# Kernel optimization log

Hardware: AMD Instinct MI355X
Metric: run time of the kernel (lower is better)

## Reference

```python
import jax, jax.numpy as jnp
import numpy as np
from jax import lax

DN = ('NCHW', 'OIHW', 'NCHW')


def squash(x):
    # x: [..., d]; squared-norm over last dim
    sq = jnp.sum(x * x, axis=-1, keepdims=True)
    return sq * x / ((1.0 + sq) * jnp.sqrt(sq))


def setup_inputs() -> dict:
    key = jax.random.key(0)
    ks = jax.random.split(key, 6)
    B = 512
    x = jax.random.normal(ks[0], (B, 1, 28, 28), dtype=jnp.float32)
    conv1_w = jax.random.normal(ks[1], (256, 1, 9, 9), dtype=jnp.float32) * 0.05
    conv1_b = jnp.zeros((256,), dtype=jnp.float32)
    conv2_w = jax.random.normal(ks[2], (256, 256, 9, 9), dtype=jnp.float32) * 0.02
    conv2_b = jnp.zeros((256,), dtype=jnp.float32)
    # W: [num_routes=1152, num_capsules=10, out_channels=16, in_channels=8]
    W = jax.random.normal(ks[3], (1152, 10, 16, 8), dtype=jnp.float32)
    return {"x": x, "conv1_w": conv1_w, "conv1_b": conv1_b,
            "conv2_w": conv2_w, "conv2_b": conv2_b, "W": W}


def reference(x, conv1_w, conv1_b, conv2_w, conv2_b, W):
    B = x.shape[0]
    # conv1 + ReLU: [B,1,28,28] -> [B,256,20,20]
    h = lax.conv_general_dilated(x, conv1_w, (1, 1), 'VALID', dimension_numbers=DN)
    h = jax.nn.relu(h + conv1_b[None, :, None, None])
    # primary capsule conv: [B,256,20,20] -> [B,256,6,6], stride 2
    h = lax.conv_general_dilated(h, conv2_w, (2, 2), 'VALID', dimension_numbers=DN)
    h = h + conv2_b[None, :, None, None]
    # reshape to capsules [B, 1152, 8] (matches torch .view on NCHW) and squash
    u = squash(h.reshape(B, -1, 8))
    # u_hat[b,r,c,o] = W[r,c,o,i] @ u[b,r,i]
    u_hat = jnp.einsum('rcoi,bri->brco', W, u)  # [B,1152,10,16]
    R, C = W.shape[0], W.shape[1]
    b_ij = jnp.zeros((R, C), dtype=x.dtype)
    num_iterations = 3
    for it in range(num_iterations):
        c_ij = jax.nn.softmax(b_ij, axis=0)          # softmax over routes
        s_j = jnp.einsum('rc,brco->bco', c_ij, u_hat)  # [B,10,16]
        v_j = squash(s_j)
        if it < num_iterations - 1:
            a_ij = jnp.einsum('brco,bco->brc', u_hat, v_j)  # agreement
            b_ij = b_ij + a_ij.mean(axis=0)
    return v_j  # [B,10,16]
```

## Files before the change

### kernel.cpp

```cpp
#include <hip/hip_runtime.h>
#include <stdint.h>


typedef unsigned short u16;
typedef unsigned int u32;
typedef _Float16 half8 __attribute__((ext_vector_type(8)));
typedef float f32x4 __attribute__((ext_vector_type(4)));

__device__ __forceinline__ u16 f2h(float f) {
  union { _Float16 h; u16 u; } cv;
  cv.h = (_Float16)f;
  return cv.u;
}

__device__ __forceinline__ void gload_lds16(const void* g, void* l) {
  __builtin_amdgcn_global_load_lds(
      (const __attribute__((address_space(1))) void*)g,
      (__attribute__((address_space(3))) void*)l, 16, 0, 0);
}

__global__ __launch_bounds__(256) void prologue_kernel(
    const float* __restrict__ x, const float* __restrict__ w1,
    const float* __restrict__ b1, const float* __restrict__ w2,
    const float* __restrict__ b2, u16* __restrict__ hT,
    u16* __restrict__ A2, float* __restrict__ u) {
  __shared__ __align__(16) char smraw[81 * 264 * 2];
  int bid = blockIdx.x;
  int tid = threadIdx.x;
  if (bid < 512) {
    float* xs = (float*)smraw;
    int b = bid;
    int co = tid;
    for (int i = co; i < 784; i += 256) xs[i] = x[(size_t)b * 784 + i];
    float w[81];
    const float* wp = w1 + co * 81;
#pragma unroll
    for (int k = 0; k < 81; ++k) w[k] = wp[k];
    float bias = b1[co];
    __syncthreads();
    u16* hb = hT + (size_t)b * 102400 + co;
    for (int yp = 0; yp < 10; ++yp) {
      int y0 = yp * 2;
      for (int g = 0; g < 5; ++g) {
        int xo = g * 4;
        float a0[4], a1[4];
#pragma unroll
        for (int j = 0; j < 4; ++j) { a0[j] = bias; a1[j] = bias; }
#pragma unroll
        for (int ky2 = 0; ky2 < 10; ++ky2) {
          const float* row = &xs[(y0 + ky2) * 28 + xo];
          float4 r0 = *(const float4*)row;
          float4 r1 = *(const float4*)(row + 4);
          float4 r2 = *(const float4*)(row + 8);
          float xr[12] = {r0.x, r0.y, r0.z, r0.w, r1.x, r1.y, r1.z, r1.w,
                          r2.x, r2.y, r2.z, r2.w};
          if (ky2 < 9) {
#pragma unroll
            for (int kx = 0; kx < 9; ++kx) {
              float wv = w[ky2 * 9 + kx];
              a0[0] = fmaf(wv, xr[kx], a0[0]);
              a0[1] = fmaf(wv, xr[kx + 1], a0[1]);
              a0[2] = fmaf(wv, xr[kx + 2], a0[2]);
              a0[3] = fmaf(wv, xr[kx + 3], a0[3]);
            }
          }
          if (ky2 >= 1) {
#pragma unroll
            for (int kx = 0; kx < 9; ++kx) {
              float wv = w[(ky2 - 1) * 9 + kx];
              a1[0] = fmaf(wv, xr[kx], a1[0]);
              a1[1] = fmaf(wv, xr[kx + 1], a1[1]);
              a1[2] = fmaf(wv, xr[kx + 2], a1[2]);
              a1[3] = fmaf(wv, xr[kx + 3], a1[3]);
            }
          }
        }
#pragma unroll
        for (int j = 0; j < 4; ++j) {
          hb[(y0 * 20 + xo + j) * 256] = f2h(fmaxf(a0[j], 0.f));
          hb[((y0 + 1) * 20 + xo + j) * 256] = f2h(fmaxf(a1[j], 0.f));
        }
      }
    }
  } else if (bid < 768) {
    u16* tl = (u16*)smraw;
    int co = bid - 512;
    const float* wp = w2 + (size_t)co * 20736;
#pragma unroll
    for (int k = 0; k < 81; ++k) {
      int li = k * 256 + tid;
      int ci = li / 81, t = li - ci * 81;
      tl[t * 264 + ci] = f2h(wp[li]);
    }
    __syncthreads();
    u16* op = A2 + (size_t)co * 20736;
    for (int oc = tid; oc < 2592; oc += 256) {
      int k0 = oc * 8;
      int t = k0 >> 8, ci0 = k0 & 255;
      *(uint4*)(op + k0) = *(const uint4*)&tl[t * 264 + ci0];
    }
  } else {
    int i = (bid - 768) * 256 + tid;
    int b = i / 2304, j0 = (i - b * 2304) * 4;
    float4 v;
    v.x = b2[j0 / 36]; v.y = b2[(j0 + 1) / 36];
    v.z = b2[(j0 + 2) / 36]; v.w = b2[(j0 + 3) / 36];
    *(float4*)(u + (size_t)b * 9216 + j0) = v;
  }
}

__global__ __launch_bounds__(512, 2) void conv2_kernel(
    const u16* __restrict__ hT, const u16* __restrict__ A2,
    float* __restrict__ u) {
  __shared__ __align__(16) u16 lds_[65536];
  char* const ldsc = (char*)lds_;
  const int bx = blockIdx.x;
  const int nbk = bx % 72, kz = bx / 72;
  const int n0 = nbk * 256;
  const int tid = threadIdx.x;
  const int lane = tid & 63, w = tid >> 6;
  const int wr = w >> 2, wc = w & 3;
  const int fr = lane & 15, fg = lane >> 4;
  const int w1024 = w * 1024;

  const int rA = tid >> 3;
  const int qsrc = (tid & 7) ^ (rA & 7);
  const int AbaseT = rA * 20736 + qsrc * 8;
  int Bb[4];
#pragma unroll
  for (int rg = 0; rg < 4; ++rg) {
    int n = n0 + rg * 64 + rA;
    int b = n / 36, sp = n - b * 36, oh = sp / 6, ow = sp - oh * 6;
    Bb[rg] = (b * 400 + oh * 40 + ow * 2) * 256 + qsrc * 8;
  }

  const int kx0 = (fg ^ (fr & 7)) << 4;
  const int kx1 = ((4 + fg) ^ (fr & 7)) << 4;
  const int wr16384 = wr * 16384;
  const int bh16384 = 32768 + (wc >> 1) * 16384;
  const int brow0 = (wc & 1) * 64;

  f32x4 acc[8][4] = {};
  half8 areg[4][2], breg[2][2][2];

#define STAGE_A(E, H, GT) do {                                               \
    char* p0_ = ldsc + (E) * 65536 + (H) * 8192 + w1024;                     \
    gload_lds16(A2 + AbaseT + (H) * 1327104 + (GT) * 64, p0_);               \
    char* p1_ = ldsc + (E) * 65536 + 16384 + (H) * 8192 + w1024;             \
    gload_lds16(A2 + AbaseT + (2 + (H)) * 1327104 + (GT) * 64, p1_);         \
  } while (0)
#define STAGE_B(E, H, BOFF) do {                                             \
    char* p_ = ldsc + (E) * 65536 + 32768 + (H) * 16384 + w1024;             \
    gload_lds16(hT + Bb[(H) * 2 + 0] + (BOFF), p_);                          \
    gload_lds16(hT + Bb[(H) * 2 + 1] + (BOFF), p_ + 8192);                   \
  } while (0)
#define RD_A(D, MH) do { _Pragma("unroll")                                   \
    for (int mr = 0; mr < 4; ++mr) {                                         \
      const char* r_ = ldsc + (D) * 65536 + wr16384 +                        \
                       ((MH) * 64 + mr * 16 + fr) * 128;                     \
      areg[mr][0] = *(const half8*)(r_ + kx0);                               \
      areg[mr][1] = *(const half8*)(r_ + kx1);                               \
    } } while (0)
#define RD_B(D, NH) do { _Pragma("unroll")                                   \
    for (int nr = 0; nr < 2; ++nr) {                                         \
      const char* r_ = ldsc + (D) * 65536 + bh16384 +                        \
                       (brow0 + (NH) * 32 + nr * 16 + fr) * 128;             \
      breg[NH][nr][0] = *(const half8*)(r_ + kx0);                           \
      breg[NH][nr][1] = *(const half8*)(r_ + kx1);                           \
    } } while (0)
#define MM16(MH, NH) do {                                                    \
    __builtin_amdgcn_s_setprio(1);                                           \
    _Pragma("unroll") for (int mr = 0; mr < 4; ++mr)                         \
    _Pragma("unroll") for (int nr = 0; nr < 2; ++nr) {                       \
      acc[(MH)*4+mr][(NH)*2+nr] = __builtin_amdgcn_mfma_f32_16x16x32_f16(    \
          areg[mr][0], breg[NH][nr][0], acc[(MH)*4+mr][(NH)*2+nr], 0, 0, 0); \
      acc[(MH)*4+mr][(NH)*2+nr] = __builtin_amdgcn_mfma_f32_16x16x32_f16(    \
          areg[mr][1], breg[NH][nr][1], acc[(MH)*4+mr][(NH)*2+nr], 0, 0, 0); \
    }                                                                        \
    __builtin_amdgcn_s_setprio(0);                                           \
  } while (0)
#define LGKM() do {                                                          \
    asm volatile("s_waitcnt lgkmcnt(0)" ::: "memory");                       \
    __builtin_amdgcn_sched_barrier(0);                                       \
  } while (0)
#define VM_BAR(N) do {                                                       \
    asm volatile("s_waitcnt vmcnt(" N ")" ::: "memory");                     \
    __builtin_amdgcn_s_barrier();                                            \
    asm volatile("" ::: "memory");                                           \
  } while (0)
#define TILE_STD2(T, D, E) do {                                              \
    const int gt_ = kz * 108 + (T) + 1;                                      \
    int tap_ = gt_ >> 2;                                                     \
    int kh_ = tap_ / 9, kw_ = tap_ - kh_ * 9;                                \
    int bo_ = (kh_ * 20 + kw_) * 256 + (gt_ & 3) * 64;                       \
    RD_A(D, 0); RD_B(D, 0); RD_B(D, 1);                                      \
    STAGE_A(E, 0, gt_); STAGE_B(E, 0, bo_); STAGE_B(E, 1, bo_);              \
    LGKM(); MM16(0, 0); MM16(0, 1); VM_BAR("6");                             \
    RD_A(D, 1);                                                              \
    STAGE_A(E, 1, gt_);                                                      \
    LGKM(); MM16(1, 0); MM16(1, 1); VM_BAR("2");                             \
  } while (0)
#define TILE_LAST2(D) do {                                                   \
    RD_A(D, 0); RD_B(D, 0); RD_B(D, 1);                                      \
    LGKM(); MM16(0, 0); MM16(0, 1); VM_BAR("0");                             \
    RD_A(D, 1);                                                              \
    LGKM(); MM16(1, 0); MM16(1, 1);                                          \
  } while (0)

  {
    const int gt0 = kz * 108;
    int tap = gt0 >> 2;
    int kh = tap / 9, kw = tap - kh * 9;
    int bo0 = (kh * 20 + kw) * 256 + (gt0 & 3) * 64;
    STAGE_A(0, 0, gt0); STAGE_B(0, 0, bo0); STAGE_B(0, 1, bo0);
    STAGE_A(0, 1, gt0);
    asm volatile("s_waitcnt vmcnt(2)" ::: "memory");
    __builtin_amdgcn_s_barrier();
    asm volatile("" ::: "memory");
  }
  for (int tt = 0; tt < 53; ++tt) {
    TILE_STD2(2 * tt, 0, 1);
    TILE_STD2(2 * tt + 1, 1, 0);
  }
  TILE_STD2(106, 0, 1);
  TILE_LAST2(1);

#pragma unroll
  for (int nf = 0; nf < 4; ++nf) {
    int cn = n0 + wc * 64 + nf * 16 + fr;
    int ob = cn / 36;
    int os = cn - ob * 36;
    float* op = u + (size_t)ob * 9216 + os;
#pragma unroll
    for (int mf = 0; mf < 8; ++mf) {
      int row0 = wr * 128 + mf * 16 + fg * 4;
#pragma unroll
      for (int qq = 0; qq < 4; ++qq)
        atomicAdd(op + (row0 + qq) * 36, acc[mf][nf][qq]);
    }
  }
#undef STAGE_A
#undef STAGE_B
#undef RD_A
#undef RD_B
#undef MM16
#undef LGKM
#undef VM_BAR
#undef TILE_STD2
#undef TILE_LAST2
}

__global__ __launch_bounds__(256) void squash_kernel(
    float* __restrict__ u, u16* __restrict__ ub) {
  int idx = blockIdx.x * 256 + threadIdx.x;
  float* up = u + (size_t)idx * 8;
  float4 a = *(const float4*)up;
  float4 c = *(const float4*)(up + 4);
  float sq = a.x * a.x + a.y * a.y + a.z * a.z + a.w * a.w +
             c.x * c.x + c.y * c.y + c.z * c.z + c.w * c.w;
  float f = sqrtf(sq) / (1.0f + sq);
  a.x *= f; a.y *= f; a.z *= f; a.w *= f;
  c.x *= f; c.y *= f; c.z *= f; c.w *= f;
  *(float4*)up = a;
  *(float4*)(up + 4) = c;
  u16 o[8];
  o[0] = f2h(a.x); o[1] = f2h(a.y); o[2] = f2h(a.z); o[3] = f2h(a.w);
  o[4] = f2h(c.x); o[5] = f2h(c.y); o[6] = f2h(c.z); o[7] = f2h(c.w);
  *(uint4*)(ub + (size_t)idx * 8) = *(uint4*)o;
}

__global__ __launch_bounds__(256) void transp_kernel(
    const u16* __restrict__ ub, u16* __restrict__ ubT) {
  __shared__ u16 tl[64][72];
  int ri0 = blockIdx.x * 64, b0 = blockIdx.y * 64;
  int tid = threadIdx.x;
  int br = tid >> 2, cq = tid & 3;
  const u16* ip = ub + (size_t)(b0 + br) * 9216 + ri0 + cq * 16;
  uint4 v0 = *(const uint4*)ip;
  uint4 v1 = *(const uint4*)(ip + 8);
  *(uint4*)&tl[br][cq * 16] = v0;
  *(uint4*)&tl[br][cq * 16 + 8] = v1;
  __syncthreads();
  int rr = tid >> 2, cb = tid & 3;
  u16 o0[8], o1[8];
#pragma unroll
  for (int j = 0; j < 8; ++j) {
    o0[j] = tl[cb * 16 + j][rr];
    o1[j] = tl[cb * 16 + 8 + j][rr];
  }
  u16* opp = ubT + (size_t)(ri0 + rr) * 512 + b0 + cb * 16;
  *(uint4*)opp = *(uint4*)o0;
  *(uint4*)(opp + 8) = *(uint4*)o1;
}

__global__ __launch_bounds__(256) void softmax_c_kernel(
    const float* __restrict__ bij, float* __restrict__ cT) {
  int c = blockIdx.x;
  int tid = threadIdx.x;
  __shared__ float red[256];
  float mx = -1e30f;
  for (int r = tid; r < 1152; r += 256) mx = fmaxf(mx, bij[r * 10 + c]);
  red[tid] = mx;
  __syncthreads();
  for (int s = 128; s > 0; s >>= 1) {
    if (tid < s) red[tid] = fmaxf(red[tid], red[tid + s]);
    __syncthreads();
  }
  mx = red[0];
  __syncthreads();
  float sum = 0.f;
  for (int r = tid; r < 1152; r += 256) sum += expf(bij[r * 10 + c] - mx);
  red[tid] = sum;
  __syncthreads();
  for (int s = 128; s > 0; s >>= 1) {
    if (tid < s) red[tid] += red[tid + s];
    __syncthreads();
  }
  float inv = 1.0f / red[0];
  for (int r = tid; r < 1152; r += 256)
    cT[c * 1152 + r] = expf(bij[r * 10 + c] - mx) * inv;
}

__global__ __launch_bounds__(256) void gemm_s_kernel(
    const float* __restrict__ W, const float* __restrict__ cT,
    const u16* __restrict__ ub, float* __restrict__ s) {
  __shared__ __align__(16) u16 Asl[160 * 72];
  __shared__ __align__(16) u16 Bsl[64 * 72];
  int nb = blockIdx.x & 7, kzi = blockIdx.x >> 3;
  int n0 = nb * 64, k0 = kzi * 256;
  int tid = threadIdx.x;
  int lane = tid & 63, wave = tid >> 6;
  int fr = lane & 15, fg = lane >> 4;

  f32x4 acc[10] = {};
#pragma unroll
  for (int st = 0; st < 4; ++st) {
    int kb = k0 + st * 64;
    __syncthreads();
#pragma unroll
    for (int j = 0; j < 5; ++j) {
      int c5 = tid + j * 256;
      int row = c5 >> 3, qq = c5 & 7;
      int cls = row >> 4, o = row & 15;
      int r = (kb + qq * 8) >> 3;
      const float* wp = W + (size_t)r * 1280 + cls * 128 + o * 8;
      float4 w0 = *(const float4*)wp;
      float4 w1 = *(const float4*)(wp + 4);
      float cs = cT[cls * 1152 + r] * 512.0f;
      u16 ov[8];
      ov[0] = f2h(w0.x * cs); ov[1] = f2h(w0.y * cs);
      ov[2] = f2h(w0.z * cs); ov[3] = f2h(w0.w * cs);
      ov[4] = f2h(w1.x * cs); ov[5] = f2h(w1.y * cs);
      ov[6] = f2h(w1.z * cs); ov[7] = f2h(w1.w * cs);
      *(uint4*)((char*)Asl + row * 144 + qq * 16) = *(uint4*)ov;
    }
#pragma unroll
    for (int j = 0; j < 2; ++j) {
      int c2 = tid + j * 256;
      int row = c2 >> 3, qq = c2 & 7;
      *(uint4*)((char*)Bsl + row * 144 + qq * 16) =
          *(const uint4*)(ub + (size_t)(n0 + row) * 9216 + kb + qq * 8);
    }
    __syncthreads();
#pragma unroll
    for (int s2 = 0; s2 < 2; ++s2) {
      int xg = (s2 * 4 + fg) * 16;
      half8 bf0 = *(const half8*)((char*)Bsl + (wave * 16 + fr) * 144 + xg);
#pragma unroll
      for (int m = 0; m < 10; ++m) {
        half8 af = *(const half8*)((char*)Asl + (m * 16 + fr) * 144 + xg);
        acc[m] = __builtin_amdgcn_mfma_f32_16x16x32_f16(af, bf0, acc[m], 0, 0, 0);
      }
    }
  }
  int bcol = n0 + wave * 16 + fr;
#pragma unroll
  for (int m = 0; m < 10; ++m)
#pragma unroll
    for (int qq = 0; qq < 4; ++qq)
      atomicAdd(s + (m * 16 + fg * 4 + qq) * 512 + bcol, acc[m][qq]);
}

__global__ __launch_bounds__(256) void squash_v_kernel(
    float* __restrict__ s, u16* __restrict__ vb) {
  int idx = blockIdx.x * 256 + threadIdx.x;
  int c = idx >> 9, b = idx & 511;
  float vals[16];
  float sq = 0.f;
#pragma unroll
  for (int o = 0; o < 16; ++o) {
    float v = s[(c * 16 + o) * 512 + b] * (1.0f / 512.0f);
    vals[o] = v;
    sq += v * v;
  }
#pragma unroll
  for (int o = 0; o < 16; ++o) s[(c * 16 + o) * 512 + b] = 0.f;
  float f = sqrtf(sq) / (1.0f + sq);
#pragma unroll
  for (int o = 0; o < 16; ++o)
    vb[(c * 16 + o) * 512 + b] = f2h(vals[o] * f * 4096.0f);
}

__global__ __launch_bounds__(256) void gemm_gc_kernel(
    const u16* __restrict__ vb, const u16* __restrict__ ubT,
    const float* __restrict__ W, float* __restrict__ bij) {
  __shared__ __align__(16) u16 Agl[160 * 72];
  __shared__ __align__(16) u16 Bgl[128 * 72];
  __shared__ float Gl[160 * 129];
  int nb = blockIdx.x % 72, kzi = blockIdx.x / 72;
  int n0 = nb * 128, k0 = kzi * 128;
  int tid = threadIdx.x;
  int lane = tid & 63, wave = tid >> 6;
  int fr = lane & 15, fg = lane >> 4;
  f32x4 acc[10][2] = {};
#pragma unroll
  for (int st = 0; st < 2; ++st) {
    int kb = k0 + st * 64;
    __syncthreads();
#pragma unroll
    for (int j = 0; j < 5; ++j) {
      int c5 = tid + j * 256;
      int row = c5 >> 3, qq = c5 & 7;
      *(uint4*)((char*)Agl + row * 144 + qq * 16) =
          *(const uint4*)(vb + (size_t)row * 512 + kb + qq * 8);
    }
#pragma unroll
    for (int j = 0; j < 4; ++j) {
      int c4 = tid + j * 256;
      int row = c4 >> 3, qq = c4 & 7;
      *(uint4*)((char*)Bgl + row * 144 + qq * 16) =
          *(const uint4*)(ubT + (size_t)(n0 + row) * 512 + kb + qq * 8);
    }
    __syncthreads();
#pragma unroll
    for (int s2 = 0; s2 < 2; ++s2) {
      int xg = (s2 * 4 + fg) * 16;
      half8 bfv[2];
#pragma unroll
      for (int nn = 0; nn < 2; ++nn)
        bfv[nn] = *(const half8*)((char*)Bgl + (wave * 32 + nn * 16 + fr) * 144 + xg);
#pragma unroll
      for (int m = 0; m < 10; ++m) {
        half8 af = *(const half8*)((char*)Agl + (m * 16 + fr) * 144 + xg);
#pragma unroll
        for (int nn = 0; nn < 2; ++nn)
          acc[m][nn] = __builtin_amdgcn_mfma_f32_16x16x32_f16(af, bfv[nn],
                                                             acc[m][nn], 0, 0, 0);
      }
    }
  }
#pragma unroll
  for (int m = 0; m < 10; ++m)
#pragma unroll
    for (int nn = 0; nn < 2; ++nn) {
      int col = wave * 32 + nn * 16 + fr;
#pragma unroll
      for (int qq = 0; qq < 4; ++qq)
        Gl[(m * 16 + fg * 4 + qq) * 129 + col] = acc[m][nn][qq];
    }
  __syncthreads();
  if (tid < 160) {
    int rl = tid / 10, c = tid - rl * 10;
    int r = (n0 >> 3) + rl;
    const float* wp = W + (size_t)r * 1280 + c * 128;
    float a = 0.f;
#pragma unroll 4
    for (int o = 0; o < 16; ++o) {
      const float* gp = &Gl[(c * 16 + o) * 129 + rl * 8];
#pragma unroll
      for (int i = 0; i < 8; ++i) a = fmaf(wp[o * 8 + i], gp[i], a);
    }
    atomicAdd(&bij[r * 10 + c], a * (1.0f / (512.0f * 4096.0f)));
  }
}

__global__ __launch_bounds__(256) void route_final_kernel(
    const float* __restrict__ cT, const float* __restrict__ u,
    const float* __restrict__ W, float* __restrict__ outp) {
  int c = blockIdx.y, b0 = blockIdx.x * 16;
  int tid = threadIdx.x, lb = tid >> 4, o = tid & 15;
  __shared__ float us[16][32][8];
  __shared__ float cs[32];
  float acc = 0.f;
  for (int r0 = 0; r0 < 1152; r0 += 32) {
    __syncthreads();
#pragma unroll
    for (int j = 0; j < 4; ++j) {
      int i4 = tid + j * 256;
      int bb = i4 >> 6, rem = i4 & 63;
      int rr = rem >> 1, hf = rem & 1;
      *(float4*)&us[bb][rr][hf * 4] =
          *(const float4*)&u[(size_t)(b0 + bb) * 9216 + (r0 + rr) * 8 + hf * 4];
    }
    if (tid < 32) cs[tid] = cT[c * 1152 + r0 + tid];
    __syncthreads();
#pragma unroll 4
    for (int rr = 0; rr < 32; ++rr) {
      const float* wp = W + ((size_t)(r0 + rr) * 10 + c) * 128 + o * 8;
      float4 w0 = *(const float4*)wp;
      float4 w1v = *(const float4*)(wp + 4);
      float4 ua = *(const float4*)&us[lb][rr][0];
      float4 ub4 = *(const float4*)&us[lb][rr][4];
      float d = w0.x * ua.x + w0.y * ua.y + w0.z * ua.z + w0.w * ua.w +
                w1v.x * ub4.x + w1v.y * ub4.y + w1v.z * ub4.z + w1v.w * ub4.w;
      acc = fmaf(cs[rr], d, acc);
    }
  }
  float sq = acc * acc;
  sq += __shfl_xor(sq, 1, 64);
  sq += __shfl_xor(sq, 2, 64);
  sq += __shfl_xor(sq, 4, 64);
  sq += __shfl_xor(sq, 8, 64);
  float f = sqrtf(sq) / (1.0f + sq);
  outp[((size_t)(b0 + lb) * 10 + c) * 16 + o] = acc * f;
}

extern "C" void kernel_launch(void* const* d_in, const int* in_sizes, int n_in,
                              void* d_out, int out_size, void* d_ws, size_t ws_size,
                              hipStream_t stream) {
  const float* x  = (const float*)d_in[0];
  const float* w1 = (const float*)d_in[1];
  const float* b1 = (const float*)d_in[2];
  const float* w2 = (const float*)d_in[3];
  const float* b2 = (const float*)d_in[4];
  const float* W  = (const float*)d_in[5];
  char* ws = (char*)d_ws;
  u16*   hT  = (u16*)ws;
  u16*   A2  = (u16*)(ws + 104857600);
  float* u   = (float*)(ws + 115474432);
  float* bij = (float*)(ws + 134348800);
  float* cT  = (float*)(ws + 134394880);
  float* s   = (float*)(ws + 134440960);
  u16*   ub  = (u16*)ws;
  u16*   ubT = (u16*)(ws + 9437184);
  u16*   vb  = (u16*)(ws + 21823488);
  float* out = (float*)d_out;

  hipMemsetAsync(bij, 0, 46080, stream);
  hipMemsetAsync(s, 0, 327680, stream);
  prologue_kernel<<<5376, 256, 0, stream>>>(x, w1, b1, w2, b2, hT, A2, u);
  conv2_kernel<<<216, 512, 0, stream>>>(hT, A2, u);
  squash_kernel<<<2304, 256, 0, stream>>>(u, ub);
  transp_kernel<<<dim3(144, 8), 256, 0, stream>>>(ub, ubT);
  for (int it = 0; it < 3; ++it) {
    softmax_c_kernel<<<10, 256, 0, stream>>>(bij, cT);
    if (it < 2) {
      gemm_s_kernel<<<288, 256, 0, stream>>>(W, cT, ub, s);
      squash_v_kernel<<<20, 256, 0, stream>>>(s, vb);
      gemm_gc_kernel<<<288, 256, 0, stream>>>(vb, ubT, W, bij);
    } else {
      route_final_kernel<<<dim3(32, 10), 256, 0, stream>>>(cT, u, W, out);
    }
  }
}
```

Baseline: 613.8 us.

## Double conv2 workgroup to 1024 threads with smaller per-wave tiles

The conv2 implicit GEMM moves from 512 to 1024 threads per block. Each of the 16 waves now computes a 64x64 output tile with 4x4 accumulators instead of 128x64, and each thread stages four 16-byte loads per K tile. The split two-phase pipeline with partial vmcnt waits is replaced by a simpler one that waits for all loads (vmcnt(0)) before each barrier. The aim is more waves for latency hiding and lower register pressure per wave. The cost is less MFMA work per LDS read and fully serialized waits on global loads at every tile.

Result: no change. 614.4 us (+0.1%).

```diff
diff --git a/kernel.cpp b/kernel.cpp
--- a/kernel.cpp
+++ b/kernel.cpp
@@ -109,7 +109,7 @@
   }
 }
 
-__global__ __launch_bounds__(512, 2) void conv2_kernel(
+__global__ __launch_bounds__(1024, 4) void conv2_kernel(
     const u16* __restrict__ hT, const u16* __restrict__ A2,
     float* __restrict__ u) {
   __shared__ __align__(16) u16 lds_[65536];
@@ -124,106 +124,86 @@
   const int w1024 = w * 1024;
 
   const int rA = tid >> 3;
-  const int qsrc = (tid & 7) ^ (rA & 7);
-  const int AbaseT = rA * 20736 + qsrc * 8;
-  int Bb[4];
-#pragma unroll
-  for (int rg = 0; rg < 4; ++rg) {
-    int n = n0 + rg * 64 + rA;
+  const int qs = (tid & 7) ^ (rA & 7);
+  const int Aoff0 = rA * 20736 + qs * 8;
+  const int Aoff1 = (128 + rA) * 20736 + qs * 8;
+  int Bb0, Bb1;
+  {
+    int n = n0 + rA;
     int b = n / 36, sp = n - b * 36, oh = sp / 6, ow = sp - oh * 6;
-    Bb[rg] = (b * 400 + oh * 40 + ow * 2) * 256 + qsrc * 8;
+    Bb0 = (b * 400 + oh * 40 + ow * 2) * 256 + qs * 8;
+    n = n0 + 128 + rA;
+    b = n / 36; sp = n - b * 36; oh = sp / 6; ow = sp - oh * 6;
+    Bb1 = (b * 400 + oh * 40 + ow * 2) * 256 + qs * 8;
   }
 
   const int kx0 = (fg ^ (fr & 7)) << 4;
   const int kx1 = ((4 + fg) ^ (fr & 7)) << 4;
-  const int wr16384 = wr * 16384;
-  const int bh16384 = 32768 + (wc >> 1) * 16384;
-  const int brow0 = (wc & 1) * 64;
-
-  f32x4 acc[8][4] = {};
-  half8 areg[4][2], breg[2][2][2];
-
-#define STAGE_A(E, H, GT) do {                                               \
-    char* p0_ = ldsc + (E) * 65536 + (H) * 8192 + w1024;                     \
-    gload_lds16(A2 + AbaseT + (H) * 1327104 + (GT) * 64, p0_);               \
-    char* p1_ = ldsc + (E) * 65536 + 16384 + (H) * 8192 + w1024;             \
-    gload_lds16(A2 + AbaseT + (2 + (H)) * 1327104 + (GT) * 64, p1_);         \
-  } while (0)
-#define STAGE_B(E, H, BOFF) do {                                             \
-    char* p_ = ldsc + (E) * 65536 + 32768 + (H) * 16384 + w1024;             \
-    gload_lds16(hT + Bb[(H) * 2 + 0] + (BOFF), p_);                          \
-    gload_lds16(hT + Bb[(H) * 2 + 1] + (BOFF), p_ + 8192);                   \
-  } while (0)
-#define RD_A(D, MH) do { _Pragma("unroll")                                   \
-    for (int mr = 0; mr < 4; ++mr) {                                         \
-      const char* r_ = ldsc + (D) * 65536 + wr16384 +                        \
-                       ((MH) * 64 + mr * 16 + fr) * 128;                     \
-      areg[mr][0] = *(const half8*)(r_ + kx0);                               \
-      areg[mr][1] = *(const half8*)(r_ + kx1);                               \
-    } } while (0)
-#define RD_B(D, NH) do { _Pragma("unroll")                                   \
-    for (int nr = 0; nr < 2; ++nr) {                                         \
-      const char* r_ = ldsc + (D) * 65536 + bh16384 +                        \
-                       (brow0 + (NH) * 32 + nr * 16 + fr) * 128;             \
-      breg[NH][nr][0] = *(const half8*)(r_ + kx0);                           \
-      breg[NH][nr][1] = *(const half8*)(r_ + kx1);                           \
-    } } while (0)
-#define MM16(MH, NH) do {                                                    \
+  const int arow = wr * 64 + fr;
+  const int brow = wc * 64 + fr;
+
+  f32x4 acc[4][4] = {};
+  half8 areg[4], breg[4];
+
+#define STAGE4(E, GT) do {                                                   \
+    int tap_ = (GT) >> 2;                                                    \
+    int kh_ = tap_ / 9, kw_ = tap_ - kh_ * 9;                                \
+    int bo_ = (kh_ * 20 + kw_) * 256 + ((GT) & 3) * 64;                      \
+    char* base_ = ldsc + (E) * 65536;                                        \
+    gload_lds16(A2 + Aoff0 + (GT) * 64, base_ + w1024);                      \
+    gload_lds16(A2 + Aoff1 + (GT) * 64, base_ + 16384 + w1024);              \
+    gload_lds16(hT + Bb0 + bo_, base_ + 32768 + w1024);                      \
+    gload_lds16(hT + Bb1 + bo_, base_ + 49152 + w1024);                      \
+  } while (0)
+#define RD8(D, KX) do { _Pragma("unroll")                                    \
+    for (int mr = 0; mr < 4; ++mr)                                           \
+      areg[mr] = *(const half8*)(ldsc + (D) * 65536 +                        \
+                                 (arow + mr * 16) * 128 + (KX));             \
+    _Pragma("unroll")                                                        \
+    for (int nr = 0; nr < 4; ++nr)                                           \
+      breg[nr] = *(const half8*)(ldsc + (D) * 65536 + 32768 +                \
+                                 (brow + nr * 16) * 128 + (KX));             \
+  } while (0)
+#define MM16() do {                                                          \
     __builtin_amdgcn_s_setprio(1);                                           \
     _Pragma("unroll") for (int mr = 0; mr < 4; ++mr)                         \
-    _Pragma("unroll") for (int nr = 0; nr < 2; ++nr) {                       \
-      acc[(MH)*4+mr][(NH)*2+nr] = __builtin_amdgcn_mfma_f32_16x16x32_f16(    \
-          areg[mr][0], breg[NH][nr][0], acc[(MH)*4+mr][(NH)*2+nr], 0, 0, 0); \
-      acc[(MH)*4+mr][(NH)*2+nr] = __builtin_amdgcn_mfma_f32_16x16x32_f16(    \
-          areg[mr][1], breg[NH][nr][1], acc[(MH)*4+mr][(NH)*2+nr], 0, 0, 0); \
-    }                                                                        \
+    _Pragma("unroll") for (int nr = 0; nr < 4; ++nr)                         \
+      acc[mr][nr] = __builtin_amdgcn_mfma_f32_16x16x32_f16(                  \
+          areg[mr], breg[nr], acc[mr][nr], 0, 0, 0);                         \
     __builtin_amdgcn_s_setprio(0);                                           \
   } while (0)
 #define LGKM() do {                                                          \
     asm volatile("s_waitcnt lgkmcnt(0)" ::: "memory");                       \
     __builtin_amdgcn_sched_barrier(0);                                       \
   } while (0)
-#define VM_BAR(N) do {                                                       \
-    asm volatile("s_waitcnt vmcnt(" N ")" ::: "memory");                     \
+#define VM_BAR0() do {                                                       \
+    asm volatile("s_waitcnt vmcnt(0)" ::: "memory");                         \
     __builtin_amdgcn_s_barrier();                                            \
     asm volatile("" ::: "memory");                                           \
   } while (0)
-#define TILE_STD2(T, D, E) do {                                              \
-    const int gt_ = kz * 108 + (T) + 1;                                      \
-    int tap_ = gt_ >> 2;                                                     \
-    int kh_ = tap_ / 9, kw_ = tap_ - kh_ * 9;                                \
-    int bo_ = (kh_ * 20 + kw_) * 256 + (gt_ & 3) * 64;                       \
-    RD_A(D, 0); RD_B(D, 0); RD_B(D, 1);                                      \
-    STAGE_A(E, 0, gt_); STAGE_B(E, 0, bo_); STAGE_B(E, 1, bo_);              \
-    LGKM(); MM16(0, 0); MM16(0, 1); VM_BAR("6");                             \
-    RD_A(D, 1);                                                              \
-    STAGE_A(E, 1, gt_);                                                      \
-    LGKM(); MM16(1, 0); MM16(1, 1); VM_BAR("2");                             \
-  } while (0)
-#define TILE_LAST2(D) do {                                                   \
-    RD_A(D, 0); RD_B(D, 0); RD_B(D, 1);                                      \
-    LGKM(); MM16(0, 0); MM16(0, 1); VM_BAR("0");                             \
-    RD_A(D, 1);                                                              \
-    LGKM(); MM16(1, 0); MM16(1, 1);                                          \
-  } while (0)
-
-  {
-    const int gt0 = kz * 108;
-    int tap = gt0 >> 2;
-    int kh = tap / 9, kw = tap - kh * 9;
-    int bo0 = (kh * 20 + kw) * 256 + (gt0 & 3) * 64;
-    STAGE_A(0, 0, gt0); STAGE_B(0, 0, bo0); STAGE_B(0, 1, bo0);
-    STAGE_A(0, 1, gt0);
-    asm volatile("s_waitcnt vmcnt(2)" ::: "memory");
-    __builtin_amdgcn_s_barrier();
-    asm volatile("" ::: "memory");
-  }
+#define TILE_STD(T, D, E) do {                                               \
+    RD8(D, kx0);                                                             \
+    STAGE4(E, kz * 108 + (T) + 1);                                           \
+    LGKM(); MM16();                                                          \
+    RD8(D, kx1); LGKM(); MM16();                                             \
+    VM_BAR0();                                                               \
+  } while (0)
+#define TILE_LAST(D) do {                                                    \
+    RD8(D, kx0); LGKM(); MM16();                                             \
+    RD8(D, kx1); LGKM(); MM16();                                             \
+  } while (0)
+
+  STAGE4(0, kz * 108);
+  asm volatile("s_waitcnt vmcnt(0)" ::: "memory");
+  __builtin_amdgcn_s_barrier();
+  asm volatile("" ::: "memory");
+
   for (int tt = 0; tt < 53; ++tt) {
-    TILE_STD2(2 * tt, 0, 1);
-    TILE_STD2(2 * tt + 1, 1, 0);
-  }
-  TILE_STD2(106, 0, 1);
-  TILE_LAST2(1);
+    TILE_STD(2 * tt, 0, 1);
+    TILE_STD(2 * tt + 1, 1, 0);
+  }
+  TILE_STD(106, 0, 1);
+  TILE_LAST(1);
 
 #pragma unroll
   for (int nf = 0; nf < 4; ++nf) {
@@ -232,22 +212,20 @@
     int os = cn - ob * 36;
     float* op = u + (size_t)ob * 9216 + os;
 #pragma unroll
-    for (int mf = 0; mf < 8; ++mf) {
-      int row0 = wr * 128 + mf * 16 + fg * 4;
+    for (int mf = 0; mf < 4; ++mf) {
+      int row0 = wr * 64 + mf * 16 + fg * 4;
 #pragma unroll
       for (int qq = 0; qq < 4; ++qq)
         atomicAdd(op + (row0 + qq) * 36, acc[mf][nf][qq]);
     }
   }
-#undef STAGE_A
-#undef STAGE_B
-#undef RD_A
-#undef RD_B
+#undef STAGE4
+#undef RD8
 #undef MM16
 #undef LGKM
-#undef VM_BAR
-#undef TILE_STD2
-#undef TILE_LAST2
+#undef VM_BAR0
+#undef TILE_STD
+#undef TILE_LAST
 }
 
 __global__ __launch_bounds__(256) void squash_kernel(
@@ -539,7 +517,7 @@
   hipMemsetAsync(bij, 0, 46080, stream);
   hipMemsetAsync(s, 0, 327680, stream);
   prologue_kernel<<<5376, 256, 0, stream>>>(x, w1, b1, w2, b2, hT, A2, u);
-  conv2_kernel<<<216, 512, 0, stream>>>(hT, A2, u);
+  conv2_kernel<<<216, 1024, 0, stream>>>(hT, A2, u);
   squash_kernel<<<2304, 256, 0, stream>>>(u, ub);
   transp_kernel<<<dim3(144, 8), 256, 0, stream>>>(ub, ubT);
   for (int it = 0; it < 3; ++it) {
```
